# Performance work log

Hardware: AMD Instinct MI355X
Metric: run time of the kernel (lower is better)

Reference implementation:

```python
import jax, jax.numpy as jnp
import numpy as np

N_NODES = 40000
N_EDGES = 640000
IN_CH = 128
HID_CH = 128
OUT_CH = 121


def setup_inputs() -> dict:
    key = jax.random.key(0)
    ks = jax.random.split(key, 6)
    x = jax.random.normal(ks[0], (N_NODES, IN_CH), dtype=jnp.float32)
    edge_index = jax.random.randint(ks[1], (2, N_EDGES), 0, N_NODES, dtype=jnp.int64)

    def xavier(k, shape):
        fan_out, fan_in = shape
        lim = np.sqrt(6.0 / (fan_in + fan_out)).astype(np.float32)
        return jax.random.uniform(k, shape, jnp.float32, -lim, lim)

    W1l = xavier(ks[2], (HID_CH, IN_CH))
    W1r = xavier(ks[3], (HID_CH, IN_CH))
    W2l = xavier(ks[4], (OUT_CH, HID_CH))
    W2r = xavier(ks[5], (OUT_CH, HID_CH))
    b1l = jnp.zeros((HID_CH,), jnp.float32)
    b1r = jnp.zeros((HID_CH,), jnp.float32)
    b2l = jnp.zeros((OUT_CH,), jnp.float32)
    b2r = jnp.zeros((OUT_CH,), jnp.float32)
    return {"x": x, "edge_index": edge_index,
            "W1l": W1l, "b1l": b1l, "W1r": W1r, "b1r": b1r,
            "W2l": W2l, "b2l": b2l, "W2r": W2r, "b2r": b2r}


def _sage_conv(h, src, dst, Wl, bl, Wr, br):
    # mean aggregation of source-node features onto destinations
    msg = h[src]                                             # [E, C]
    agg = jax.ops.segment_sum(msg, dst, num_segments=N_NODES)
    cnt = jax.ops.segment_sum(jnp.ones((src.shape[0],), h.dtype), dst,
                              num_segments=N_NODES)
    agg = agg / jnp.maximum(cnt, 1.0)[:, None]
    # out = lin_l(agg) + lin_r(h)
    return agg @ Wl.T + bl + h @ Wr.T + br


def reference(x, edge_index, W1l, b1l, W1r, b1r, W2l, b2l, W2r, b2r):
    src, dst = edge_index[0], edge_index[1]
    h = jax.nn.relu(_sage_conv(x, src, dst, W1l, b1l, W1r, b1r))
    # dropout is identity in inference mode
    return _sage_conv(h, src, dst, W2l, b2l, W2r, b2r)
```

## Files before the change

### kernel.cpp

```cpp
#include <hip/hip_runtime.h>
#include <hip/hip_fp8.h>


#define NCH 128
#define CAPX 12
#define EPT 8

typedef __bf16 bf16x8 __attribute__((ext_vector_type(8)));
typedef float f32x4 __attribute__((ext_vector_type(4)));
typedef float f32x2 __attribute__((ext_vector_type(2)));
typedef unsigned int u32x4 __attribute__((ext_vector_type(4)));
typedef unsigned int u32x2 __attribute__((ext_vector_type(2)));
typedef unsigned short u16x8 __attribute__((ext_vector_type(8)));
typedef float f32x4v __attribute__((ext_vector_type(4)));

static __device__ __forceinline__ unsigned short f2b(float f) {
  return __builtin_bit_cast(unsigned short, static_cast<__bf16>(f));
}
static __device__ __forceinline__ unsigned char f2q_hw(float f) {
  return (unsigned char)(__builtin_amdgcn_cvt_pk_fp8_f32(f, f, 0u, false) & 0xffu);
}

__global__ __launch_bounds__(256) void k_main(
    const int* __restrict__ src, const int* __restrict__ dst, int E,
    int* __restrict__ cntx, unsigned short* __restrict__ slotu,
    int* __restrict__ ovf_n, int2* __restrict__ ovf,
    const float* __restrict__ x, unsigned short* __restrict__ xb,
    unsigned char* __restrict__ x8, int n8,
    const float* __restrict__ W1l, const float* __restrict__ W1r,
    const float* __restrict__ b1l, const float* __restrict__ b1r,
    const float* __restrict__ W2l, const float* __restrict__ W2r,
    const float* __restrict__ b2l, const float* __restrict__ b2r,
    unsigned short* __restrict__ pack1, unsigned short* __restrict__ pack2,
    float* __restrict__ bsum1, float* __restrict__ bsum2, int NOUT,
    int nbBkt, int nbCvt, int Nn) {
  int blk = blockIdx.x;
  if (blk < nbBkt) {
    unsigned int xcc;
    asm volatile("s_getreg_b32 %0, hwreg(HW_REG_XCC_ID)" : "=s"(xcc));
    xcc &= 7u;
    const long cbase = (long)xcc * Nn;
    const long lbase = (long)xcc * Nn * CAPX;
    const int base = blk * (256 * EPT) + (int)threadIdx.x;
    int d[EPT], s[EPT], pos[EPT];
#pragma unroll
    for (int j = 0; j < EPT; ++j) {
      const int e = base + j * 256;
      const bool ok = e < E;
      d[j] = ok ? __builtin_nontemporal_load(dst + e) : -1;
      s[j] = ok ? __builtin_nontemporal_load(src + e) : 0;
    }
#pragma unroll
    for (int j = 0; j < EPT; ++j) {
      pos[j] = (d[j] >= 0)
          ? __hip_atomic_fetch_add(&cntx[cbase + d[j]], 1,
                                   __ATOMIC_RELAXED, __HIP_MEMORY_SCOPE_WORKGROUP)
          : 0;
    }
#pragma unroll
    for (int j = 0; j < EPT; ++j) {
      if (d[j] >= 0) {
        if (pos[j] < CAPX)
          slotu[lbase + (long)d[j] * CAPX + pos[j]] = (unsigned short)s[j];
        else {
          int o = atomicAdd(ovf_n, 1);
          ovf[o] = make_int2(d[j], s[j]);
        }
      }
    }
    return;
  }
  blk -= nbBkt;
  if (blk < nbCvt) {
    int i = blk * 256 + threadIdx.x;
    if (i < n8) {
      const f32x4v va = __builtin_nontemporal_load((const f32x4v*)x + 2 * i);
      const f32x4v vb = __builtin_nontemporal_load((const f32x4v*)x + 2 * i + 1);
      u16x8 r;
      r[0] = f2b(va.x); r[1] = f2b(va.y); r[2] = f2b(va.z); r[3] = f2b(va.w);
      r[4] = f2b(vb.x); r[5] = f2b(vb.y); r[6] = f2b(vb.z); r[7] = f2b(vb.w);
      *((u16x8*)xb + i) = r;
      unsigned int w0 = 0u, w1 = 0u;
      w0 = __builtin_amdgcn_cvt_pk_fp8_f32(va.x, va.y, w0, false);
      w0 = __builtin_amdgcn_cvt_pk_fp8_f32(va.z, va.w, w0, true);
      w1 = __builtin_amdgcn_cvt_pk_fp8_f32(vb.x, vb.y, w1, false);
      w1 = __builtin_amdgcn_cvt_pk_fp8_f32(vb.z, vb.w, w1, true);
      u32x2 u; u[0] = w0; u[1] = w1;
      *((u32x2*)x8 + i) = u;
    }
    return;
  }
  blk -= nbCvt;
  const int layer = blk >> 4;
  const float* Wl = layer ? W2l : W1l;
  const float* Wr = layer ? W2r : W1r;
  const float* bl = layer ? b2l : b1l;
  const float* br = layer ? b2r : b1r;
  unsigned short* pack = layer ? pack2 : pack1;
  float* bsum = layer ? bsum2 : bsum1;
  const int NO = layer ? NOUT : NCH;
  int tid = (blk & 15) * 256 + threadIdx.x;
  int c = tid >> 9;
  int t = (tid >> 6) & 7;
  int l = tid & 63;
  int n = t * 16 + (l & 15);
  int kb = c * 32 + ((l >> 4) << 3);
  unsigned short o[8];
#pragma unroll
  for (int j = 0; j < 8; ++j) {
    int k = kb + j;
    float v = 0.f;
    if (n < NO) v = (k < 128) ? Wl[n * 128 + k] : Wr[n * 128 + (k - 128)];
    o[j] = f2b(v);
  }
  ushort4 lo, hi;
  lo.x = o[0]; lo.y = o[1]; lo.z = o[2]; lo.w = o[3];
  hi.x = o[4]; hi.y = o[5]; hi.z = o[6]; hi.w = o[7];
  *(ushort4*)(pack + (long)tid * 8) = lo;
  *(ushort4*)(pack + (long)tid * 8 + 4) = hi;
  if (tid < 128) bsum[tid] = (tid < NO) ? (bl[tid] + br[tid]) : 0.f;
}

__global__ __launch_bounds__(256) void k_agg(
    const unsigned char* __restrict__ feat8, const int* __restrict__ cntx,
    const unsigned short* __restrict__ slotu, const int* __restrict__ ovf_n,
    const int2* __restrict__ ovf, unsigned short* __restrict__ agg, int N) {
  __shared__ unsigned short list[32][104];
  __shared__ int degs[32], ms[32];
  __shared__ int cnts[32][9];
  const int lg = threadIdx.x >> 3;
  const int ln = threadIdx.x & 7;
  const int g = blockIdx.x * 32 + lg;

  {
    const int xx = threadIdx.x >> 5;
    const int lgg = threadIdx.x & 31;
    const int gg = blockIdx.x * 32 + lgg;
    cnts[lgg][xx] = (gg < N) ? cntx[(long)xx * N + gg] : 0;
  }
  __syncthreads();

  if (g < N) {
    int deg = 0, p = 0, myoff = 0, mycc = 0;
#pragma unroll
    for (int xx = 0; xx < 8; ++xx) {
      const int cv = cnts[lg][xx];
      const int cc = (cv < CAPX) ? cv : CAPX;
      if (ln == xx) { myoff = p; mycc = cc; }
      p += cc;
      deg += cv;
    }
    if (ln == 0) { degs[lg] = deg; ms[lg] = p; }
    const unsigned short* sp = slotu + ((long)ln * N + g) * CAPX;
    for (int i = 0; i < mycc; ++i) list[lg][myoff + i] = sp[i];
  } else if (ln == 0) {
    degs[lg] = 0; ms[lg] = 0;
  }
  __syncthreads();

  if (g >= N) return;
  const int m = ms[lg];
  const int col = ln * 16;
  const unsigned char* fcol = feat8 + col;

  f32x2 acc[8];
#pragma unroll
  for (int k = 0; k < 8; ++k) acc[k] = (f32x2){0.f, 0.f};

#define ACC_ROW(W)                                                        \
  do {                                                                    \
    _Pragma("unroll")                                                     \
    for (int q = 0; q < 4; ++q) {                                         \
      acc[2 * q + 0] += __builtin_amdgcn_cvt_pk_f32_fp8((W)[q], false);   \
      acc[2 * q + 1] += __builtin_amdgcn_cvt_pk_f32_fp8((W)[q], true);    \
    }                                                                     \
  } while (0)

  const unsigned short* __restrict__ il = list[lg];
  int j = 0;
  for (; j + 7 < m; j += 8) {
    const int i0 = il[j + 0], i1 = il[j + 1], i2 = il[j + 2], i3 = il[j + 3];
    const int i4 = il[j + 4], i5 = il[j + 5], i6 = il[j + 6], i7 = il[j + 7];
    const u32x4 w0 = *(const u32x4*)(fcol + (long)i0 * NCH);
    const u32x4 w1 = *(const u32x4*)(fcol + (long)i1 * NCH);
    const u32x4 w2 = *(const u32x4*)(fcol + (long)i2 * NCH);
    const u32x4 w3 = *(const u32x4*)(fcol + (long)i3 * NCH);
    const u32x4 w4 = *(const u32x4*)(fcol + (long)i4 * NCH);
    const u32x4 w5 = *(const u32x4*)(fcol + (long)i5 * NCH);
    const u32x4 w6 = *(const u32x4*)(fcol + (long)i6 * NCH);
    const u32x4 w7 = *(const u32x4*)(fcol + (long)i7 * NCH);
    ACC_ROW(w0); ACC_ROW(w1); ACC_ROW(w2); ACC_ROW(w3);
    ACC_ROW(w4); ACC_ROW(w5); ACC_ROW(w6); ACC_ROW(w7);
  }
  if (j + 3 < m) {
    const int i0 = il[j + 0], i1 = il[j + 1], i2 = il[j + 2], i3 = il[j + 3];
    const u32x4 w0 = *(const u32x4*)(fcol + (long)i0 * NCH);
    const u32x4 w1 = *(const u32x4*)(fcol + (long)i1 * NCH);
    const u32x4 w2 = *(const u32x4*)(fcol + (long)i2 * NCH);
    const u32x4 w3 = *(const u32x4*)(fcol + (long)i3 * NCH);
    ACC_ROW(w0); ACC_ROW(w1); ACC_ROW(w2); ACC_ROW(w3);
    j += 4;
  }
  for (; j < m; ++j) {
    const u32x4 w = *(const u32x4*)(fcol + (long)il[j] * NCH);
    ACC_ROW(w);
  }

  const int on = *ovf_n;
  for (int o = 0; o < on; ++o) {
    const int2 p = ovf[o];
    if (p.x == g) {
      const u32x4 w = *(const u32x4*)(fcol + (long)p.y * NCH);
      ACC_ROW(w);
    }
  }
#undef ACC_ROW

  const int deg = degs[lg];
  const int dd = (deg < 1) ? 1 : deg;
  const float inv = 1.f / (float)dd;
  u16x8 r0, r1;
#pragma unroll
  for (int k = 0; k < 8; ++k) {
    r0[k] = f2b(acc[k >> 1][k & 1] * inv);
    r1[k] = f2b(acc[4 + (k >> 1)][k & 1] * inv);
  }
  *(u16x8*)(agg + (long)g * NCH + col) = r0;
  *(u16x8*)(agg + (long)g * NCH + col + 8) = r1;
}

__global__ __launch_bounds__(256) void k_gemm(
    const unsigned short* __restrict__ Ag,
    const unsigned short* __restrict__ Sf,
    const unsigned short* __restrict__ pack,
    const float* __restrict__ bsum,
    unsigned short* __restrict__ outb,
    unsigned char* __restrict__ out8,
    float* __restrict__ outf,
    int M, int NO, int do_relu) {
  const int wave = threadIdx.x >> 6;
  const int lane = threadIdx.x & 63;
  const int R = blockIdx.x * 128 + wave * 32;
  const int mrow = lane & 15;
  const int koct = (lane >> 4) * 8;

  int r0 = R + mrow;       if (r0 > M - 1) r0 = M - 1;
  int r1 = R + 16 + mrow;  if (r1 > M - 1) r1 = M - 1;

  f32x4 acc[2][8];
#pragma unroll
  for (int mt = 0; mt < 2; ++mt)
#pragma unroll
    for (int t = 0; t < 8; ++t) acc[mt][t] = (f32x4){0.f, 0.f, 0.f, 0.f};

#pragma unroll
  for (int c = 0; c < 8; ++c) {
    const unsigned short* __restrict__ Abase = (c < 4) ? Ag : Sf;
    const int k0 = (c & 3) * 32;
    const bf16x8 a0 = *(const bf16x8*)(Abase + (long)r0 * NCH + k0 + koct);
    const bf16x8 a1 = *(const bf16x8*)(Abase + (long)r1 * NCH + k0 + koct);
    const unsigned short* bp = pack + ((long)(c * 8) * 64 + lane) * 8;
#pragma unroll
    for (int t = 0; t < 8; ++t) {
      const bf16x8 bfrag = *(const bf16x8*)(bp + (long)t * 512);
      acc[0][t] = __builtin_amdgcn_mfma_f32_16x16x32_bf16(a0, bfrag, acc[0][t], 0, 0, 0);
      acc[1][t] = __builtin_amdgcn_mfma_f32_16x16x32_bf16(a1, bfrag, acc[1][t], 0, 0, 0);
    }
  }

  const int nloc = lane & 15;
  const int rquad = (lane >> 4) * 4;
#pragma unroll
  for (int mt = 0; mt < 2; ++mt) {
#pragma unroll
    for (int t = 0; t < 8; ++t) {
      const int n = t * 16 + nloc;
      const float bias = bsum[n];
#pragma unroll
      for (int r = 0; r < 4; ++r) {
        const int m = R + mt * 16 + rquad + r;
        if (m < M && n < NO) {
          float v = acc[mt][t][r] + bias;
          if (do_relu) v = fmaxf(v, 0.f);
          if (outb) {
            outb[(long)m * NCH + n] = f2b(v);
            out8[(long)m * NCH + n] = f2q_hw(v);
          } else {
            outf[(long)m * NO + n] = v;
          }
        }
      }
    }
  }
}


extern "C" void kernel_launch(void* const* d_in, const int* in_sizes, int n_in,
                              void* d_out, int out_size, void* d_ws, size_t ws_size,
                              hipStream_t stream) {
  const float* x = (const float*)d_in[0];
  const int* ei = (const int*)d_in[1];
  const float* W1l = (const float*)d_in[2];
  const float* b1l = (const float*)d_in[3];
  const float* W1r = (const float*)d_in[4];
  const float* b1r = (const float*)d_in[5];
  const float* W2l = (const float*)d_in[6];
  const float* b2l = (const float*)d_in[7];
  const float* W2r = (const float*)d_in[8];
  const float* b2r = (const float*)d_in[9];
  float* out = (float*)d_out;

  const int N = in_sizes[0] / NCH;
  const int E = in_sizes[1] / 2;
  const int NOUT = out_size / N;

  const int* src = ei;
  const int* dst = ei + E;

  char* w = (char*)d_ws;
  auto alloc = [&](size_t bytes) {
    char* p = w;
    w += (bytes + 255) & ~(size_t)255;
    return p;
  };
  unsigned short* xb = (unsigned short*)alloc((size_t)N * NCH * 2);
  unsigned short* hb = (unsigned short*)alloc((size_t)N * NCH * 2);
  unsigned short* aggb = (unsigned short*)alloc((size_t)N * NCH * 2);
  unsigned char* x8 = (unsigned char*)alloc((size_t)N * NCH);
  unsigned char* h8 = (unsigned char*)alloc((size_t)N * NCH);
  unsigned short* pack1 = (unsigned short*)alloc(8 * 8 * 64 * 8 * 2);
  unsigned short* pack2 = (unsigned short*)alloc(8 * 8 * 64 * 8 * 2);
  float* bsum1 = (float*)alloc(128 * 4);
  float* bsum2 = (float*)alloc(128 * 4);
  int* cntx = (int*)alloc(((size_t)N * 8 + 4) * 4);
  int* ovf_n = cntx + (size_t)N * 8;
  unsigned short* slotu = (unsigned short*)alloc((size_t)N * 8 * CAPX * 2);
  int2* ovf = (int2*)alloc((size_t)E * 8);

  const int n8 = N * NCH / 8;
  const int nbBkt = (E + 256 * EPT - 1) / (256 * EPT);
  const int nbCvt = (n8 + 255) / 256;

  hipMemsetAsync(cntx, 0, ((size_t)N * 8 + 4) * 4, stream);

  k_main<<<nbBkt + nbCvt + 32, 256, 0, stream>>>(
      src, dst, E, cntx, slotu, ovf_n, ovf,
      x, xb, x8, n8,
      W1l, W1r, b1l, b1r, W2l, W2r, b2l, b2r,
      pack1, pack2, bsum1, bsum2, NOUT, nbBkt, nbCvt, N);

  const int gaggr = (N + 31) / 32;
  const int gblk = (N + 127) / 128;

  k_agg<<<gaggr, 256, 0, stream>>>(x8, cntx, slotu, ovf_n, ovf, aggb, N);
  k_gemm<<<gblk, 256, 0, stream>>>(aggb, xb, pack1, bsum1, hb, h8,
                                   (float*)nullptr, N, NCH, 1);
  k_agg<<<gaggr, 256, 0, stream>>>(h8, cntx, slotu, ovf_n, ovf, aggb, N);
  k_gemm<<<gblk, 256, 0, stream>>>(aggb, hb, pack2, bsum2,
                                   (unsigned short*)nullptr, (unsigned char*)nullptr,
                                   out, N, NOUT, 0);
}
```

Baseline: 189.5 us.

## Fuse neighbor aggregation and dual-weight GEMM into one kernel per layer

Merges the aggregation kernel and the MFMA GEMM kernel into a single kernel per SAGE layer. Each 32-node block first writes its mean-aggregated rows, then after a block barrier its four waves each compute two 16-column output tiles over the same 32 rows. This removes two launches and the inter-kernel gap, and the aggregated rows are read back while likely still in cache. In exchange, each block now does only 32 rows of GEMM, so B fragments are reloaded from global by four times as many blocks, and the GEMM phase cannot overlap other blocks' gathers as cleanly.

```diff
diff --git a/kernel.cpp b/kernel.cpp
--- a/kernel.cpp
+++ b/kernel.cpp
@@ -121,10 +121,18 @@
   if (tid < 128) bsum[tid] = (tid < NO) ? (bl[tid] + br[tid]) : 0.f;
 }
 
-__global__ __launch_bounds__(256) void k_agg(
+__global__ __launch_bounds__(256) void k_fused(
     const unsigned char* __restrict__ feat8, const int* __restrict__ cntx,
     const unsigned short* __restrict__ slotu, const int* __restrict__ ovf_n,
-    const int2* __restrict__ ovf, unsigned short* __restrict__ agg, int N) {
+    const int2* __restrict__ ovf,
+    unsigned short* __restrict__ aggb,
+    const unsigned short* __restrict__ Sf,
+    const unsigned short* __restrict__ pack,
+    const float* __restrict__ bsum,
+    unsigned short* __restrict__ outb,
+    unsigned char* __restrict__ out8,
+    float* __restrict__ outf,
+    int N, int NO, int do_relu) {
   __shared__ unsigned short list[32][104];
   __shared__ int degs[32], ms[32];
   __shared__ int cnts[32][9];
@@ -158,14 +166,14 @@
   }
   __syncthreads();
 
-  if (g >= N) return;
-  const int m = ms[lg];
-  const int col = ln * 16;
-  const unsigned char* fcol = feat8 + col;
-
-  f32x2 acc[8];
-#pragma unroll
-  for (int k = 0; k < 8; ++k) acc[k] = (f32x2){0.f, 0.f};
+  if (g < N) {
+    const int m = ms[lg];
+    const int col = ln * 16;
+    const unsigned char* fcol = feat8 + col;
+
+    f32x2 acc[8];
+#pragma unroll
+    for (int k = 0; k < 8; ++k) acc[k] = (f32x2){0.f, 0.f};
 
 #define ACC_ROW(W)                                                        \
   do {                                                                    \
@@ -176,95 +184,89 @@
     }                                                                     \
   } while (0)
 
-  const unsigned short* __restrict__ il = list[lg];
-  int j = 0;
-  for (; j + 7 < m; j += 8) {
-    const int i0 = il[j + 0], i1 = il[j + 1], i2 = il[j + 2], i3 = il[j + 3];
-    const int i4 = il[j + 4], i5 = il[j + 5], i6 = il[j + 6], i7 = il[j + 7];
-    const u32x4 w0 = *(const u32x4*)(fcol + (long)i0 * NCH);
-    const u32x4 w1 = *(const u32x4*)(fcol + (long)i1 * NCH);
-    const u32x4 w2 = *(const u32x4*)(fcol + (long)i2 * NCH);
-    const u32x4 w3 = *(const u32x4*)(fcol + (long)i3 * NCH);
-    const u32x4 w4 = *(const u32x4*)(fcol + (long)i4 * NCH);
-    const u32x4 w5 = *(const u32x4*)(fcol + (long)i5 * NCH);
-    const u32x4 w6 = *(const u32x4*)(fcol + (long)i6 * NCH);
-    const u32x4 w7 = *(const u32x4*)(fcol + (long)i7 * NCH);
-    ACC_ROW(w0); ACC_ROW(w1); ACC_ROW(w2); ACC_ROW(w3);
-    ACC_ROW(w4); ACC_ROW(w5); ACC_ROW(w6); ACC_ROW(w7);
-  }
-  if (j + 3 < m) {
-    const int i0 = il[j + 0], i1 = il[j + 1], i2 = il[j + 2], i3 = il[j + 3];
-    const u32x4 w0 = *(const u32x4*)(fcol + (long)i0 * NCH);
-    const u32x4 w1 = *(const u32x4*)(fcol + (long)i1 * NCH);
-    const u32x4 w2 = *(const u32x4*)(fcol + (long)i2 * NCH);
-    const u32x4 w3 = *(const u32x4*)(fcol + (long)i3 * NCH);
-    ACC_ROW(w0); ACC_ROW(w1); ACC_ROW(w2); ACC_ROW(w3);
-    j += 4;
-  }
-  for (; j < m; ++j) {
-    const u32x4 w = *(const u32x4*)(fcol + (long)il[j] * NCH);
-    ACC_ROW(w);
-  }
-
-  const int on = *ovf_n;
-  for (int o = 0; o < on; ++o) {
-    const int2 p = ovf[o];
-    if (p.x == g) {
-      const u32x4 w = *(const u32x4*)(fcol + (long)p.y * NCH);
+    const unsigned short* __restrict__ il = list[lg];
+    int j = 0;
+    for (; j + 7 < m; j += 8) {
+      const int i0 = il[j + 0], i1 = il[j + 1], i2 = il[j + 2], i3 = il[j + 3];
+      const int i4 = il[j + 4], i5 = il[j + 5], i6 = il[j + 6], i7 = il[j + 7];
+      const u32x4 w0 = *(const u32x4*)(fcol + (long)i0 * NCH);
+      const u32x4 w1 = *(const u32x4*)(fcol + (long)i1 * NCH);
+      const u32x4 w2 = *(const u32x4*)(fcol + (long)i2 * NCH);
+      const u32x4 w3 = *(const u32x4*)(fcol + (long)i3 * NCH);
+      const u32x4 w4 = *(const u32x4*)(fcol + (long)i4 * NCH);
+      const u32x4 w5 = *(const u32x4*)(fcol + (long)i5 * NCH);
+      const u32x4 w6 = *(const u32x4*)(fcol + (long)i6 * NCH);
+      const u32x4 w7 = *(const u32x4*)(fcol + (long)i7 * NCH);
+      ACC_ROW(w0); ACC_ROW(w1); ACC_ROW(w2); ACC_ROW(w3);
+      ACC_ROW(w4); ACC_ROW(w5); ACC_ROW(w6); ACC_ROW(w7);
+    }
+    if (j + 3 < m) {
+      const int i0 = il[j + 0], i1 = il[j + 1], i2 = il[j + 2], i3 = il[j + 3];
+      const u32x4 w0 = *(const u32x4*)(fcol + (long)i0 * NCH);
+      const u32x4 w1 = *(const u32x4*)(fcol + (long)i1 * NCH);
+      const u32x4 w2 = *(const u32x4*)(fcol + (long)i2 * NCH);
+      const u32x4 w3 = *(const u32x4*)(fcol + (long)i3 * NCH);
+      ACC_ROW(w0); ACC_ROW(w1); ACC_ROW(w2); ACC_ROW(w3);
+      j += 4;
+    }
+    for (; j < m; ++j) {
+      const u32x4 w = *(const u32x4*)(fcol + (long)il[j] * NCH);
       ACC_ROW(w);
     }
-  }
+
+    const int on = *ovf_n;
+    for (int o = 0; o < on; ++o) {
+      const int2 p = ovf[o];
+      if (p.x == g) {
+        const u32x4 w = *(const u32x4*)(fcol + (long)p.y * NCH);
+        ACC_ROW(w);
+      }
+    }
 #undef ACC_ROW
 
-  const int deg = degs[lg];
-  const int dd = (deg < 1) ? 1 : deg;
-  const float inv = 1.f / (float)dd;
-  u16x8 r0, r1;
-#pragma unroll
-  for (int k = 0; k < 8; ++k) {
-    r0[k] = f2b(acc[k >> 1][k & 1] * inv);
-    r1[k] = f2b(acc[4 + (k >> 1)][k & 1] * inv);
-  }
-  *(u16x8*)(agg + (long)g * NCH + col) = r0;
-  *(u16x8*)(agg + (long)g * NCH + col + 8) = r1;
-}
-
-__global__ __launch_bounds__(256) void k_gemm(
-    const unsigned short* __restrict__ Ag,
-    const unsigned short* __restrict__ Sf,
-    const unsigned short* __restrict__ pack,
-    const float* __restrict__ bsum,
-    unsigned short* __restrict__ outb,
-    unsigned char* __restrict__ out8,
-    float* __restrict__ outf,
-    int M, int NO, int do_relu) {
+    const int deg = degs[lg];
+    const int dd = (deg < 1) ? 1 : deg;
+    const float inv = 1.f / (float)dd;
+    u16x8 r0, r1;
+#pragma unroll
+    for (int k = 0; k < 8; ++k) {
+      r0[k] = f2b(acc[k >> 1][k & 1] * inv);
+      r1[k] = f2b(acc[4 + (k >> 1)][k & 1] * inv);
+    }
+    *(u16x8*)(aggb + (long)g * NCH + col) = r0;
+    *(u16x8*)(aggb + (long)g * NCH + col + 8) = r1;
+  }
+
+  __threadfence_block();
+  __syncthreads();
+
   const int wave = threadIdx.x >> 6;
   const int lane = threadIdx.x & 63;
-  const int R = blockIdx.x * 128 + wave * 32;
+  const int base = blockIdx.x * 32;
   const int mrow = lane & 15;
   const int koct = (lane >> 4) * 8;
 
-  int r0 = R + mrow;       if (r0 > M - 1) r0 = M - 1;
-  int r1 = R + 16 + mrow;  if (r1 > M - 1) r1 = M - 1;
-
-  f32x4 acc[2][8];
+  int r0 = base + mrow;       if (r0 > N - 1) r0 = N - 1;
+  int r1 = base + 16 + mrow;  if (r1 > N - 1) r1 = N - 1;
+
+  f32x4 acc2[2][2];
 #pragma unroll
   for (int mt = 0; mt < 2; ++mt)
 #pragma unroll
-    for (int t = 0; t < 8; ++t) acc[mt][t] = (f32x4){0.f, 0.f, 0.f, 0.f};
+    for (int tt = 0; tt < 2; ++tt) acc2[mt][tt] = (f32x4){0.f, 0.f, 0.f, 0.f};
 
 #pragma unroll
   for (int c = 0; c < 8; ++c) {
-    const unsigned short* __restrict__ Abase = (c < 4) ? Ag : Sf;
+    const unsigned short* __restrict__ Abase = (c < 4) ? aggb : Sf;
     const int k0 = (c & 3) * 32;
     const bf16x8 a0 = *(const bf16x8*)(Abase + (long)r0 * NCH + k0 + koct);
     const bf16x8 a1 = *(const bf16x8*)(Abase + (long)r1 * NCH + k0 + koct);
-    const unsigned short* bp = pack + ((long)(c * 8) * 64 + lane) * 8;
-#pragma unroll
-    for (int t = 0; t < 8; ++t) {
-      const bf16x8 bfrag = *(const bf16x8*)(bp + (long)t * 512);
-      acc[0][t] = __builtin_amdgcn_mfma_f32_16x16x32_bf16(a0, bfrag, acc[0][t], 0, 0, 0);
-      acc[1][t] = __builtin_amdgcn_mfma_f32_16x16x32_bf16(a1, bfrag, acc[1][t], 0, 0, 0);
+#pragma unroll
+    for (int tt = 0; tt < 2; ++tt) {
+      const int t = 2 * wave + tt;
+      const bf16x8 bfrag = *(const bf16x8*)(pack + ((long)(c * 8 + t) * 64 + lane) * 8);
+      acc2[0][tt] = __builtin_amdgcn_mfma_f32_16x16x32_bf16(a0, bfrag, acc2[0][tt], 0, 0, 0);
+      acc2[1][tt] = __builtin_amdgcn_mfma_f32_16x16x32_bf16(a1, bfrag, acc2[1][tt], 0, 0, 0);
     }
   }
 
@@ -273,14 +275,14 @@
 #pragma unroll
   for (int mt = 0; mt < 2; ++mt) {
 #pragma unroll
-    for (int t = 0; t < 8; ++t) {
-      const int n = t * 16 + nloc;
+    for (int tt = 0; tt < 2; ++tt) {
+      const int n = (2 * wave + tt) * 16 + nloc;
       const float bias = bsum[n];
 #pragma unroll
       for (int r = 0; r < 4; ++r) {
-        const int m = R + mt * 16 + rquad + r;
-        if (m < M && n < NO) {
-          float v = acc[mt][t][r] + bias;
+        const int m = base + mt * 16 + rquad + r;
+        if (m < N && n < NO) {
+          float v = acc2[mt][tt][r] + bias;
           if (do_relu) v = fmaxf(v, 0.f);
           if (outb) {
             outb[(long)m * NCH + n] = f2b(v);
@@ -349,14 +351,13 @@
       W1l, W1r, b1l, b1r, W2l, W2r, b2l, b2r,
       pack1, pack2, bsum1, bsum2, NOUT, nbBkt, nbCvt, N);
 
-  const int gaggr = (N + 31) / 32;
-  const int gblk = (N + 127) / 128;
-
-  k_agg<<<gaggr, 256, 0, stream>>>(x8, cntx, slotu, ovf_n, ovf, aggb, N);
-  k_gemm<<<gblk, 256, 0, stream>>>(aggb, xb, pack1, bsum1, hb, h8,
-                                   (float*)nullptr, N, NCH, 1);
-  k_agg<<<gaggr, 256, 0, stream>>>(h8, cntx, slotu, ovf_n, ovf, aggb, N);
-  k_gemm<<<gblk, 256, 0, stream>>>(aggb, hb, pack2, bsum2,
-                                   (unsigned short*)nullptr, (unsigned char*)nullptr,
-                                   out, N, NOUT, 0);
-}
+  const int gfused = (N + 31) / 32;
+
+  k_fused<<<gfused, 256, 0, stream>>>(x8, cntx, slotu, ovf_n, ovf, aggb, xb,
+                                      pack1, bsum1, hb, h8, (float*)nullptr,
+                                      N, NCH, 1);
+  k_fused<<<gfused, 256, 0, stream>>>(h8, cntx, slotu, ovf_n, ovf, aggb, hb,
+                                      pack2, bsum2,
+                                      (unsigned short*)nullptr, (unsigned char*)nullptr,
+                                      out, N, NOUT, 0);
+}
```

Result: slower. 193.3 us (+2.0%).
